# Kernel tuning notes

Hardware: AMD Instinct MI355X
Metric: run time of the kernel (lower is better)

The kernel has to match this reference:

```python
import jax, jax.numpy as jnp
import numpy as np

S, E, K = 100000, 30000, 1000
D, F = 64, 128
B = 16384
NNZ_S, NNZ_E, NNZ_K = 1600000, 480000, 32000
LAYERS = 3
MOMENTUM = 0.9
LEAK = 0.1


def setup_inputs() -> dict:
    key = jax.random.key(0)
    ks = jax.random.split(key, 24)
    inp = {}
    inp['student_id'] = jax.random.randint(ks[0], (B,), 0, S, dtype=jnp.int32)
    inp['exercise_id'] = jax.random.randint(ks[1], (B,), 0, E, dtype=jnp.int32)
    inp['q_mask'] = jnp.ones((B, K), jnp.float32)
    # embedding tables (xavier-ish scale)
    inp['stu_emb'] = jax.random.normal(ks[2], (S, D), jnp.float32) * 0.05
    inp['exer_emb'] = jax.random.normal(ks[3], (E, D), jnp.float32) * 0.05
    inp['know_emb'] = jax.random.normal(ks[4], (K, D), jnp.float32) * 0.05
    inp['impact_emb'] = jax.random.normal(ks[5], (E, D), jnp.float32) * 0.05
    # sparse adjacencies in COO form (rows, cols, vals); vals ~ normalized weights
    inp['s_rows'] = jax.random.randint(ks[6], (NNZ_S,), 0, S, dtype=jnp.int32)
    inp['s_cols'] = jax.random.randint(ks[7], (NNZ_S,), 0, S, dtype=jnp.int32)
    inp['s_vals'] = jax.random.uniform(ks[8], (NNZ_S,), jnp.float32) / 16.0
    inp['e_rows'] = jax.random.randint(ks[9], (NNZ_E,), 0, E, dtype=jnp.int32)
    inp['e_cols'] = jax.random.randint(ks[10], (NNZ_E,), 0, E, dtype=jnp.int32)
    inp['e_vals'] = jax.random.uniform(ks[11], (NNZ_E,), jnp.float32) / 16.0
    inp['k_rows'] = jax.random.randint(ks[12], (NNZ_K,), 0, K, dtype=jnp.int32)
    inp['k_cols'] = jax.random.randint(ks[13], (NNZ_K,), 0, K, dtype=jnp.int32)
    inp['k_vals'] = jax.random.uniform(ks[14], (NNZ_K,), jnp.float32) / 32.0
    # linear layers (stored as [in, out])
    inp['W_stu'] = jax.random.normal(ks[15], (D, F), jnp.float32) * 0.1
    inp['b_stu'] = jnp.zeros((F,), jnp.float32)
    inp['W_exer'] = jax.random.normal(ks[16], (D, F), jnp.float32) * 0.1
    inp['b_exer'] = jnp.zeros((F,), jnp.float32)
    inp['W_know'] = jax.random.normal(ks[17], (D, F), jnp.float32) * 0.1
    inp['b_know'] = jnp.zeros((F,), jnp.float32)
    inp['W_disc'] = jax.random.normal(ks[18], (D, 1), jnp.float32) * 0.1
    inp['b_disc'] = jnp.zeros((1,), jnp.float32)
    return inp


def spmm(rows, cols, vals, x, n):
    # sparse [n,n] @ dense [n,d] via gather + segment_sum
    return jax.ops.segment_sum(vals[:, None] * x[cols], rows, num_segments=n)


def convolution(emb, rows, cols, vals, n):
    # layers of SpMM with momentum residual; mean over all (layers+1) outputs
    acc = emb
    cur = emb
    for _ in range(LAYERS):
        cur = spmm(rows, cols, vals, cur, n) + MOMENTUM * cur
        acc = acc + cur
    return acc / (LAYERS + 1)


def reference(student_id, exercise_id, q_mask, stu_emb, exer_emb, know_emb,
              impact_emb, s_rows, s_cols, s_vals, e_rows, e_cols, e_vals,
              k_rows, k_cols, k_vals, W_stu, b_stu, W_exer, b_exer,
              W_know, b_know, W_disc, b_disc):
    stu_fwd = convolution(stu_emb, s_rows, s_cols, s_vals, S)    # [S, D]
    exer_fwd = convolution(exer_emb, e_rows, e_cols, e_vals, E)  # [E, D]
    know_fwd = convolution(know_emb, k_rows, k_cols, k_vals, K)  # [K, D]

    batch_student = stu_fwd[student_id]    # [B, D]
    batch_exercise = exer_fwd[exercise_id]  # [B, D]

    student_ts = jax.nn.leaky_relu(batch_student @ W_stu + b_stu, LEAK)   # [B, F]
    diff_ts = jax.nn.leaky_relu(batch_exercise @ W_exer + b_exer, LEAK)  # [B, F]
    knowledge_ts = jax.nn.leaky_relu(know_fwd @ W_know + b_know, LEAK)   # [K, F]
    disc_ts = jax.nn.sigmoid(batch_exercise @ W_disc + b_disc)          # [B, 1]

    student_ts = student_ts @ knowledge_ts.T  # [B, K]
    diff_ts = diff_ts @ knowledge_ts.T        # [B, K]
    knowledge_impact_ts = impact_emb[exercise_id]  # [B, D]
    return (student_ts, diff_ts, disc_ts, knowledge_ts, knowledge_impact_ts)
```

## Files before the change

### kernel.cpp

```cpp
#include <hip/hip_runtime.h>
#include <hip/hip_bf16.h>

#define S_N 100000
#define E_N 30000
#define K_N 1000
#define D_K 64
#define F_K 128
#define B_N 16384
#define NNZ_S 1600000
#define NNZ_E 480000
#define NNZ_K 32000
#define NNZ_TOT (NNZ_S + NNZ_E + NNZ_K)

#define NB_S 782
#define NB_E 235
#define NB_K 8
#define NB_TOT (NB_S + NB_E + NB_K)

#define CHUNK 4096
#define SB_S 391
#define SB_E 118
#define SB_K 8
#define SB_TOT (SB_S + SB_E + SB_K)

typedef __attribute__((ext_vector_type(8))) short sh8;
typedef __attribute__((ext_vector_type(4))) float f4;

__device__ inline float b2f(ushort u) { return __uint_as_float((unsigned)u << 16); }
__device__ inline ushort f2b(float f) {
    unsigned u = __float_as_uint(f);
    return (ushort)((u + 0x7fffu + ((u >> 16) & 1u)) >> 16);
}

__global__ void bucket_count(const int* __restrict__ sr, const int* __restrict__ er,
                             const int* __restrict__ kr, int* bcnt_tot) {
    int blk = blockIdx.x;
    const int* rows; int boff, nnz, nb, lblk;
    if (blk < SB_S)            { lblk = blk;              rows = sr; boff = 0;           nnz = NNZ_S; nb = NB_S; }
    else if (blk < SB_S + SB_E){ lblk = blk - SB_S;       rows = er; boff = NB_S;        nnz = NNZ_E; nb = NB_E; }
    else                       { lblk = blk - SB_S - SB_E; rows = kr; boff = NB_S + NB_E; nnz = NNZ_K; nb = NB_K; }
    __shared__ int hist[NB_S];
    int t = threadIdx.x;
    for (int i = t; i < nb; i += 256) hist[i] = 0;
    __syncthreads();
    int start = lblk * CHUNK, end = min(start + CHUNK, nnz);
    for (int i = start + t; i < end; i += 256) atomicAdd(&hist[rows[i] >> 7], 1);
    __syncthreads();
    for (int i = t; i < nb; i += 256) {
        int h = hist[i];
        if (h) atomicAdd(&bcnt_tot[boff + i], h);
    }
}

__global__ void bucket_scan(const int* __restrict__ bcnt_tot, int* bucket_base,
                            int* rp_s, int* rp_e, int* rp_k) {
    __shared__ int sd[256];
    int t = threadIdx.x;
    int v[5]; int s = 0;
    for (int j = 0; j < 5; j++) {
        int idx = t * 5 + j;
        v[j] = (idx < NB_TOT) ? bcnt_tot[idx] : 0;
        s += v[j];
    }
    sd[t] = s; __syncthreads();
    for (int off = 1; off < 256; off <<= 1) {
        int x = (t >= off) ? sd[t - off] : 0;
        __syncthreads();
        sd[t] += x;
        __syncthreads();
    }
    int pre = sd[t] - s;
    for (int j = 0; j < 5; j++) {
        int idx = t * 5 + j;
        if (idx < NB_TOT) {
            int segoff = (idx < NB_S) ? 0 : (idx < NB_S + NB_E) ? NNZ_S : (NNZ_S + NNZ_E);
            bucket_base[idx] = pre - segoff;
            pre += v[j];
        }
    }
    if (t == 0) { rp_s[S_N] = NNZ_S; rp_e[E_N] = NNZ_E; rp_k[K_N] = NNZ_K; }
}

__global__ void stage1_bin(const int* __restrict__ sr, const int* __restrict__ sc,
                           const float* __restrict__ sv,
                           const int* __restrict__ er, const int* __restrict__ ec,
                           const float* __restrict__ ev,
                           const int* __restrict__ kr, const int* __restrict__ kc,
                           const float* __restrict__ kv,
                           const int* __restrict__ bucket_base,
                           int* rsv, int2* stg_s, int2* stg_e, int2* stg_k) {
    int blk = blockIdx.x;
    const int* rows; const int* cols; const float* vals;
    int2* stg; int boff, nnz, nb, lblk;
    if (blk < SB_S) {
        lblk = blk; rows = sr; cols = sc; vals = sv; stg = stg_s;
        boff = 0; nnz = NNZ_S; nb = NB_S;
    } else if (blk < SB_S + SB_E) {
        lblk = blk - SB_S; rows = er; cols = ec; vals = ev; stg = stg_e;
        boff = NB_S; nnz = NNZ_E; nb = NB_E;
    } else {
        lblk = blk - SB_S - SB_E; rows = kr; cols = kc; vals = kv; stg = stg_k;
        boff = NB_S + NB_E; nnz = NNZ_K; nb = NB_K;
    }
    __shared__ int hist[NB_S];
    __shared__ int wbase[NB_S];
    int t = threadIdx.x;
    for (int i = t; i < nb; i += 256) hist[i] = 0;
    __syncthreads();
    int start = lblk * CHUNK, end = min(start + CHUNK, nnz);
    for (int i = start + t; i < end; i += 256) atomicAdd(&hist[rows[i] >> 7], 1);
    __syncthreads();
    for (int i = t; i < nb; i += 256) {
        int h = hist[i];
        int b0 = h ? atomicAdd(&rsv[boff + i], h) : 0;
        wbase[i] = bucket_base[boff + i] + b0;
        hist[i] = 0;
    }
    __syncthreads();
    for (int i = start + t; i < end; i += 256) {
        int r = rows[i]; int b = r >> 7;
        int p = wbase[b] + atomicAdd(&hist[b], 1);
        stg[p] = make_int2(((r & 127) << 25) | cols[i], __float_as_int(vals[i]));
    }
}

__global__ void stage2_place(const int* __restrict__ bucket_base, const int* __restrict__ bcnt_tot,
                             const int2* __restrict__ stg_s, int2* pr_s, int* rp_s,
                             const int2* __restrict__ stg_e, int2* pr_e, int* rp_e,
                             const int2* __restrict__ stg_k, int2* pr_k, int* rp_k) {
    int gb = blockIdx.x;
    int b = gb;
    const int2* stg; int2* pr; int* rp; int len;
    if (b < NB_S) { stg = stg_s; pr = pr_s; rp = rp_s; len = S_N; }
    else if (b < NB_S + NB_E) { b -= NB_S; stg = stg_e; pr = pr_e; rp = rp_e; len = E_N; }
    else { b -= NB_S + NB_E; stg = stg_k; pr = pr_k; rp = rp_k; len = K_N; }
    int r0 = b << 7;
    int rows = min(128, len - r0);
    __shared__ int cnt[128];
    __shared__ int nx[128];
    int t = threadIdx.x;
    if (t < 128) cnt[t] = 0;
    __syncthreads();
    int j0 = bucket_base[gb], j1 = j0 + bcnt_tot[gb];
    for (int j = j0 + t; j < j1; j += 256)
        atomicAdd(&cnt[((unsigned)stg[j].x) >> 25], 1);
    __syncthreads();
    int my = (t < 128) ? cnt[t] : 0;
    for (int off = 1; off < 128; off <<= 1) {
        int y = (t < 128 && t >= off) ? cnt[t - off] : 0;
        __syncthreads();
        if (t < 128) cnt[t] += y;
        __syncthreads();
    }
    if (t < 128) {
        int ex = j0 + cnt[t] - my;
        nx[t] = ex;
        if (t < rows) rp[r0 + t] = ex;
    }
    __syncthreads();
    for (int j = j0 + t; j < j1; j += 256) {
        int2 e = stg[j];
        int r_rel = ((unsigned)e.x) >> 25;
        int col = e.x & 0x01FFFFFF;
        int p = atomicAdd(&nx[r_rel], 1);
        pr[p] = make_int2(col, e.y);
    }
}

__global__ void convert_bf16(const float* __restrict__ a, const float* __restrict__ b,
                             const float* __restrict__ c,
                             ushort* oa, ushort* ob, ushort* oc) {
    const int NA = S_N * 64, NB = E_N * 64, NC = K_N * 64;
    int i = (blockIdx.x * 256 + threadIdx.x) * 4;
    const float* src; ushort* dst;
    if (i < NA) { src = a; dst = oa; }
    else if (i < NA + NB) { i -= NA; src = b; dst = ob; }
    else if (i < NA + NB + NC) { i -= NA + NB; src = c; dst = oc; }
    else return;
    float4 v = *(const float4*)&src[i];
    ushort4 o;
    o.x = f2b(v.x); o.y = f2b(v.y); o.z = f2b(v.z); o.w = f2b(v.w);
    *(ushort4*)&dst[i] = o;
}

__device__ __forceinline__ void spmm_row_compute(
        const int* __restrict__ rp, const int2* __restrict__ pr,
        const ushort* __restrict__ x, int r, int l, float* a) {
    const ushort4* __restrict__ X4 = (const ushort4*)x;
    int j0 = rp[r], j1 = rp[r + 1];
    ushort4 self = X4[r * 16 + l];
    float a0 = 0.9f * b2f(self.x), a1 = 0.9f * b2f(self.y);
    float a2 = 0.9f * b2f(self.z), a3 = 0.9f * b2f(self.w);
    int j = j0;
    for (; j + 8 <= j1; j += 8) {
        int2 q0 = pr[j + 0], q1 = pr[j + 1], q2 = pr[j + 2], q3 = pr[j + 3];
        int2 q4 = pr[j + 4], q5 = pr[j + 5], q6 = pr[j + 6], q7 = pr[j + 7];
        ushort4 v0 = X4[q0.x * 16 + l];
        ushort4 v1 = X4[q1.x * 16 + l];
        ushort4 v2 = X4[q2.x * 16 + l];
        ushort4 v3 = X4[q3.x * 16 + l];
        ushort4 v4 = X4[q4.x * 16 + l];
        ushort4 v5 = X4[q5.x * 16 + l];
        ushort4 v6 = X4[q6.x * 16 + l];
        ushort4 v7 = X4[q7.x * 16 + l];
        float w0 = __int_as_float(q0.y), w1 = __int_as_float(q1.y);
        float w2 = __int_as_float(q2.y), w3 = __int_as_float(q3.y);
        float w4 = __int_as_float(q4.y), w5 = __int_as_float(q5.y);
        float w6 = __int_as_float(q6.y), w7 = __int_as_float(q7.y);
        a0 = fmaf(w0, b2f(v0.x), a0); a1 = fmaf(w0, b2f(v0.y), a1);
        a2 = fmaf(w0, b2f(v0.z), a2); a3 = fmaf(w0, b2f(v0.w), a3);
        a0 = fmaf(w1, b2f(v1.x), a0); a1 = fmaf(w1, b2f(v1.y), a1);
        a2 = fmaf(w1, b2f(v1.z), a2); a3 = fmaf(w1, b2f(v1.w), a3);
        a0 = fmaf(w2, b2f(v2.x), a0); a1 = fmaf(w2, b2f(v2.y), a1);
        a2 = fmaf(w2, b2f(v2.z), a2); a3 = fmaf(w2, b2f(v2.w), a3);
        a0 = fmaf(w3, b2f(v3.x), a0); a1 = fmaf(w3, b2f(v3.y), a1);
        a2 = fmaf(w3, b2f(v3.z), a2); a3 = fmaf(w3, b2f(v3.w), a3);
        a0 = fmaf(w4, b2f(v4.x), a0); a1 = fmaf(w4, b2f(v4.y), a1);
        a2 = fmaf(w4, b2f(v4.z), a2); a3 = fmaf(w4, b2f(v4.w), a3);
        a0 = fmaf(w5, b2f(v5.x), a0); a1 = fmaf(w5, b2f(v5.y), a1);
        a2 = fmaf(w5, b2f(v5.z), a2); a3 = fmaf(w5, b2f(v5.w), a3);
        a0 = fmaf(w6, b2f(v6.x), a0); a1 = fmaf(w6, b2f(v6.y), a1);
        a2 = fmaf(w6, b2f(v6.z), a2); a3 = fmaf(w6, b2f(v6.w), a3);
        a0 = fmaf(w7, b2f(v7.x), a0); a1 = fmaf(w7, b2f(v7.y), a1);
        a2 = fmaf(w7, b2f(v7.z), a2); a3 = fmaf(w7, b2f(v7.w), a3);
    }
    if (j + 4 <= j1) {
        int2 q0 = pr[j + 0], q1 = pr[j + 1], q2 = pr[j + 2], q3 = pr[j + 3];
        ushort4 v0 = X4[q0.x * 16 + l];
        ushort4 v1 = X4[q1.x * 16 + l];
        ushort4 v2 = X4[q2.x * 16 + l];
        ushort4 v3 = X4[q3.x * 16 + l];
        float w0 = __int_as_float(q0.y), w1 = __int_as_float(q1.y);
        float w2 = __int_as_float(q2.y), w3 = __int_as_float(q3.y);
        a0 = fmaf(w0, b2f(v0.x), a0); a1 = fmaf(w0, b2f(v0.y), a1);
        a2 = fmaf(w0, b2f(v0.z), a2); a3 = fmaf(w0, b2f(v0.w), a3);
        a0 = fmaf(w1, b2f(v1.x), a0); a1 = fmaf(w1, b2f(v1.y), a1);
        a2 = fmaf(w1, b2f(v1.z), a2); a3 = fmaf(w1, b2f(v1.w), a3);
        a0 = fmaf(w2, b2f(v2.x), a0); a1 = fmaf(w2, b2f(v2.y), a1);
        a2 = fmaf(w2, b2f(v2.z), a2); a3 = fmaf(w2, b2f(v2.w), a3);
        a0 = fmaf(w3, b2f(v3.x), a0); a1 = fmaf(w3, b2f(v3.y), a1);
        a2 = fmaf(w3, b2f(v3.z), a2); a3 = fmaf(w3, b2f(v3.w), a3);
        j += 4;
    }
    if (j < j1) {
        int last = j1 - 1;
        int2 q0 = pr[j];
        int2 q1 = pr[min(j + 1, last)];
        int2 q2 = pr[min(j + 2, last)];
        int2 q3 = pr[min(j + 3, last)];
        ushort4 v0 = X4[q0.x * 16 + l];
        ushort4 v1 = X4[q1.x * 16 + l];
        ushort4 v2 = X4[q2.x * 16 + l];
        ushort4 v3 = X4[q3.x * 16 + l];
        float w0 = __int_as_float(q0.y);
        float w1 = (j + 1 <= last) ? __int_as_float(q1.y) : 0.f;
        float w2 = (j + 2 <= last) ? __int_as_float(q2.y) : 0.f;
        float w3 = (j + 3 <= last) ? __int_as_float(q3.y) : 0.f;
        a0 = fmaf(w0, b2f(v0.x), a0); a1 = fmaf(w0, b2f(v0.y), a1);
        a2 = fmaf(w0, b2f(v0.z), a2); a3 = fmaf(w0, b2f(v0.w), a3);
        a0 = fmaf(w1, b2f(v1.x), a0); a1 = fmaf(w1, b2f(v1.y), a1);
        a2 = fmaf(w1, b2f(v1.z), a2); a3 = fmaf(w1, b2f(v1.w), a3);
        a0 = fmaf(w2, b2f(v2.x), a0); a1 = fmaf(w2, b2f(v2.y), a1);
        a2 = fmaf(w2, b2f(v2.z), a2); a3 = fmaf(w2, b2f(v2.w), a3);
        a0 = fmaf(w3, b2f(v3.x), a0); a1 = fmaf(w3, b2f(v3.y), a1);
        a2 = fmaf(w3, b2f(v3.z), a2); a3 = fmaf(w3, b2f(v3.w), a3);
    }
    a[0] = a0; a[1] = a1; a[2] = a2; a[3] = a3;
}

__global__ void spmm_full(const int* __restrict__ rp_s, const int2* __restrict__ pr_s,
                          const ushort* __restrict__ xs, ushort* ys,
                          const int* __restrict__ rp_e, const int2* __restrict__ pr_e,
                          const ushort* __restrict__ xe, ushort* ye,
                          const int* __restrict__ rp_k, const int2* __restrict__ pr_k,
                          const ushort* __restrict__ xk, ushort* yk) {
    int w = (blockIdx.x * 256 + threadIdx.x) >> 4;
    int l = threadIdx.x & 15;
    const int* rp; const int2* pr; const ushort* x; ushort* y; int r;
    if (w < S_N) { rp = rp_s; pr = pr_s; x = xs; y = ys; r = w; }
    else if (w < S_N + E_N) { rp = rp_e; pr = pr_e; x = xe; y = ye; r = w - S_N; }
    else if (w < S_N + E_N + K_N) { rp = rp_k; pr = pr_k; x = xk; y = yk; r = w - S_N - E_N; }
    else return;
    float a[4];
    spmm_row_compute(rp, pr, x, r, l, a);
    ushort4 o;
    o.x = f2b(a[0]); o.y = f2b(a[1]); o.z = f2b(a[2]); o.w = f2b(a[3]);
    *(ushort4*)&y[r * 64 + l * 4] = o;
}

__global__ void spmm_last(const int* __restrict__ sid, const int* __restrict__ eid,
                          const int* __restrict__ rp_s, const int2* __restrict__ pr_s,
                          const ushort* __restrict__ xs, ushort* c3s,
                          const int* __restrict__ rp_e, const int2* __restrict__ pr_e,
                          const ushort* __restrict__ xe, ushort* c3e,
                          const int* __restrict__ rp_k, const int2* __restrict__ pr_k,
                          const ushort* __restrict__ xk, ushort* yk) {
    int w = (blockIdx.x * 256 + threadIdx.x) >> 4;
    int l = threadIdx.x & 15;
    const int* rp; const int2* pr; const ushort* x; ushort* y; int r; int orow;
    if (w < B_N) { rp = rp_s; pr = pr_s; x = xs; y = c3s; r = sid[w]; orow = w; }
    else if (w < 2 * B_N) {
        int b = w - B_N;
        rp = rp_e; pr = pr_e; x = xe; y = c3e; r = eid[b]; orow = b;
    } else if (w < 2 * B_N + K_N) {
        r = w - 2 * B_N;
        rp = rp_k; pr = pr_k; x = xk; y = yk; orow = r;
    } else return;
    float a[4];
    spmm_row_compute(rp, pr, x, r, l, a);
    ushort4 o;
    o.x = f2b(a[0]); o.y = f2b(a[1]); o.z = f2b(a[2]); o.w = f2b(a[3]);
    *(ushort4*)&y[orow * 64 + l * 4] = o;
}

__global__ void gather_init(const int* __restrict__ sid, const int* __restrict__ eid,
                            const float* __restrict__ src_s, const float* __restrict__ src_e,
                            const float* __restrict__ src_k,
                            float* bacc_s, float* bacc_e, float* kacc) {
    int i = blockIdx.x * 256 + threadIdx.x;
    const int BD = B_N * 64;
    if (i < BD) {
        int b = i >> 6, d = i & 63;
        bacc_s[i] = src_s[(long)sid[b] * 64 + d];
    } else if (i < 2 * BD) {
        int ii = i - BD; int b = ii >> 6, d = ii & 63;
        bacc_e[ii] = src_e[(long)eid[b] * 64 + d];
    } else if (i < 2 * BD + K_N * 64) {
        int ii = i - 2 * BD;
        kacc[ii] = src_k[ii];
    }
}

__global__ void gather_accb(const int* __restrict__ sid, const int* __restrict__ eid,
                            const ushort* __restrict__ src_s, const ushort* __restrict__ src_e,
                            const ushort* __restrict__ src_k,
                            float* bacc_s, float* bacc_e, float* kacc) {
    int i = blockIdx.x * 256 + threadIdx.x;
    const int BD = B_N * 64;
    if (i < BD) {
        int b = i >> 6, d = i & 63;
        bacc_s[i] += b2f(src_s[(long)sid[b] * 64 + d]);
    } else if (i < 2 * BD) {
        int ii = i - BD; int b = ii >> 6, d = ii & 63;
        bacc_e[ii] += b2f(src_e[(long)eid[b] * 64 + d]);
    } else if (i < 2 * BD + K_N * 64) {
        int ii = i - 2 * BD;
        kacc[ii] += b2f(src_k[ii]);
    }
}

__global__ void dense_mm(const float* __restrict__ bacc_s, const ushort* __restrict__ c3_s,
                         const float* __restrict__ bacc_e, const ushort* __restrict__ c3_e,
                         const float* __restrict__ W_stu, const float* __restrict__ b_stu,
                         const float* __restrict__ W_exer, const float* __restrict__ b_exer,
                         __hip_bfloat16* st_b, __hip_bfloat16* df_b) {
    int which = blockIdx.y;
    const float* bacc = which ? bacc_e : bacc_s;
    const ushort* c3 = which ? c3_e : c3_s;
    const float* W = which ? W_exer : W_stu;
    const float* bias = which ? b_exer : b_stu;
    __hip_bfloat16* out = which ? df_b : st_b;
    int r0 = blockIdx.x * 2;
    int t = threadIdx.x;
    __shared__ float X[2][64];
    if (t < 128) {
        int lr = t >> 6, d = t & 63; int b = r0 + lr;
        X[lr][d] = 0.25f * (bacc[(long)b * 64 + d] + b2f(c3[(long)b * 64 + d]));
    }
    __syncthreads();
    int lr = t >> 7, f = t & 127;
    float acc = bias[f];
    for (int d = 0; d < 64; d++) acc += X[lr][d] * W[d * 128 + f];
    acc = acc > 0.f ? acc : 0.1f * acc;
    out[(long)(r0 + lr) * 128 + f] = __float2bfloat16(acc);
}

__global__ void know_mm(const float* __restrict__ kacc, const ushort* __restrict__ cur3_k,
                        const float* __restrict__ W, const float* __restrict__ bias,
                        float* out_f32, __hip_bfloat16* kn_b) {
    int r0 = blockIdx.x * 2;
    int t = threadIdx.x;
    __shared__ float X[2][64];
    if (t < 128) {
        int lr = t >> 6, d = t & 63; int r = r0 + lr;
        X[lr][d] = (r < K_N) ? 0.25f * (kacc[r * 64 + d] + b2f(cur3_k[r * 64 + d])) : 0.f;
    }
    __syncthreads();
    int lr = t >> 7, f = t & 127; int r = r0 + lr;
    float acc = bias[f];
    for (int d = 0; d < 64; d++) acc += X[lr][d] * W[d * 128 + f];
    acc = acc > 0.f ? acc : 0.1f * acc;
    if (r < K_N) {
        out_f32[(long)r * 128 + f] = acc;
        kn_b[(long)r * 128 + f] = __float2bfloat16(acc);
    } else {
        kn_b[(long)r * 128 + f] = __float2bfloat16(0.f);
    }
}

__global__ void disc_kernel(const float* __restrict__ bacc_e, const ushort* __restrict__ c3_e,
                            const float* __restrict__ W_disc, const float* __restrict__ b_disc,
                            float* out) {
    int w = (blockIdx.x * 256 + threadIdx.x) >> 6;
    int d = threadIdx.x & 63;
    if (w >= B_N) return;
    float x = 0.25f * (bacc_e[(long)w * 64 + d] + b2f(c3_e[(long)w * 64 + d])) * W_disc[d];
    for (int off = 32; off > 0; off >>= 1) x += __shfl_down(x, off, 64);
    if (d == 0) {
        float z = x + b_disc[0];
        out[w] = 1.f / (1.f + expf(-z));
    }
}

__global__ void impact_kernel(const int* __restrict__ eid, const float* __restrict__ imp,
                              float* out) {
    int i = blockIdx.x * 256 + threadIdx.x;
    if (i >= B_N * 64) return;
    int b = i >> 6, d = i & 63;
    out[i] = imp[(long)eid[b] * 64 + d];
}

__global__ void big_mm(const __hip_bfloat16* __restrict__ st, const __hip_bfloat16* __restrict__ df,
                       const __hip_bfloat16* __restrict__ kn,
                       float* __restrict__ out0, float* __restrict__ out1) {
    const ushort* X = (const ushort*)(blockIdx.z ? df : st);
    const ushort* Kn = (const ushort*)kn;
    float* out = blockIdx.z ? out1 : out0;
    int wv = threadIdx.x >> 6;
    int lane = threadIdx.x & 63;
    int m_blk = blockIdx.y * 64 + (wv >> 1) * 32;
    int n_blk = blockIdx.x * 64 + (wv & 1) * 32;
    int q = lane >> 4, l16 = lane & 15;
    f4 acc00 = {0.f, 0.f, 0.f, 0.f}, acc01 = acc00, acc10 = acc00, acc11 = acc00;
    for (int s = 0; s < 4; s++) {
        int kofs = s * 32 + q * 8;
        sh8 a0 = *(const sh8*)&X[(long)(m_blk + l16) * 128 + kofs];
        sh8 a1 = *(const sh8*)&X[(long)(m_blk + 16 + l16) * 128 + kofs];
        sh8 b0 = *(const sh8*)&Kn[(long)(n_blk + l16) * 128 + kofs];
        sh8 b1 = *(const sh8*)&Kn[(long)(n_blk + 16 + l16) * 128 + kofs];
        acc00 = __builtin_amdgcn_mfma_f32_16x16x32_bf16(a0, b0, acc00, 0, 0, 0);
        acc01 = __builtin_amdgcn_mfma_f32_16x16x32_bf16(a0, b1, acc01, 0, 0, 0);
        acc10 = __builtin_amdgcn_mfma_f32_16x16x32_bf16(a1, b0, acc10, 0, 0, 0);
        acc11 = __builtin_amdgcn_mfma_f32_16x16x32_bf16(a1, b1, acc11, 0, 0, 0);
    }
    for (int r = 0; r < 4; r++) {
        int row0 = m_blk + q * 4 + r;
        int row1 = m_blk + 16 + q * 4 + r;
        int col0 = n_blk + l16;
        int col1 = n_blk + 16 + l16;
        if (col0 < K_N) {
            out[(long)row0 * K_N + col0] = acc00[r];
            out[(long)row1 * K_N + col0] = acc10[r];
        }
        if (col1 < K_N) {
            out[(long)row0 * K_N + col1] = acc01[r];
            out[(long)row1 * K_N + col1] = acc11[r];
        }
    }
}

extern "C" void kernel_launch(void* const* d_in, const int* in_sizes, int n_in,
                              void* d_out, int out_size, void* d_ws, size_t ws_size,
                              hipStream_t stream) {
    const int* sid = (const int*)d_in[0];
    const int* eid = (const int*)d_in[1];
    const float* stu_emb = (const float*)d_in[3];
    const float* exer_emb = (const float*)d_in[4];
    const float* know_emb = (const float*)d_in[5];
    const float* impact_emb = (const float*)d_in[6];
    const int* s_rows = (const int*)d_in[7];
    const int* s_cols = (const int*)d_in[8];
    const float* s_vals = (const float*)d_in[9];
    const int* e_rows = (const int*)d_in[10];
    const int* e_cols = (const int*)d_in[11];
    const float* e_vals = (const float*)d_in[12];
    const int* k_rows = (const int*)d_in[13];
    const int* k_cols = (const int*)d_in[14];
    const float* k_vals = (const float*)d_in[15];
    const float* W_stu = (const float*)d_in[16];
    const float* b_stu = (const float*)d_in[17];
    const float* W_exer = (const float*)d_in[18];
    const float* b_exer = (const float*)d_in[19];
    const float* W_know = (const float*)d_in[20];
    const float* b_know = (const float*)d_in[21];
    const float* W_disc = (const float*)d_in[22];
    const float* b_disc = (const float*)d_in[23];

    float* out = (float*)d_out;
    float* out_st = out;
    float* out_df = out + 16384000;
    float* out_disc = out + 32768000;
    float* out_kn = out + 32784384;
    float* out_imp = out + 32912384;

    char* p = (char*)d_ws;
    auto alloc = [&](size_t bytes) -> char* {
        char* r = p;
        p += (bytes + 255) & ~(size_t)255;
        return r;
    };
    ushort* xb_s = (ushort*)alloc((size_t)S_N * 64 * 2);
    ushort* xb_e = (ushort*)alloc((size_t)E_N * 64 * 2);
    ushort* xb_k = (ushort*)alloc((size_t)K_N * 64 * 2);
    ushort* bufA_s = (ushort*)alloc((size_t)S_N * 64 * 2);
    ushort* bufB_s = (ushort*)alloc((size_t)S_N * 64 * 2);
    ushort* bufA_e = (ushort*)alloc((size_t)E_N * 64 * 2);
    ushort* bufB_e = (ushort*)alloc((size_t)E_N * 64 * 2);
    ushort* bufA_k = (ushort*)alloc((size_t)K_N * 64 * 2);
    ushort* bufB_k = (ushort*)alloc((size_t)K_N * 64 * 2);
    ushort* c3s = (ushort*)alloc((size_t)B_N * 64 * 2);
    ushort* c3e = (ushort*)alloc((size_t)B_N * 64 * 2);
    float* bacc_s = (float*)alloc((size_t)B_N * 64 * 4);
    float* bacc_e = (float*)alloc((size_t)B_N * 64 * 4);
    float* kacc = (float*)alloc((size_t)K_N * 64 * 4);
    __hip_bfloat16* st_b = (__hip_bfloat16*)alloc((size_t)B_N * 128 * 2);
    __hip_bfloat16* df_b = (__hip_bfloat16*)alloc((size_t)B_N * 128 * 2);
    __hip_bfloat16* kn_b = (__hip_bfloat16*)alloc((size_t)1024 * 128 * 2);
    int* bcnt_tot = (int*)alloc((size_t)2 * NB_TOT * 4);
    int* rsv = bcnt_tot + NB_TOT;
    int* bucket_base = (int*)alloc((size_t)NB_TOT * 4);
    int* rp_s = (int*)alloc((size_t)(S_N + 1) * 4);
    int* rp_e = (int*)alloc((size_t)(E_N + 1) * 4);
    int* rp_k = (int*)alloc((size_t)(K_N + 1) * 4);
    int2* stg_s = (int2*)alloc((size_t)NNZ_S * 8);
    int2* stg_e = (int2*)alloc((size_t)NNZ_E * 8);
    int2* stg_k = (int2*)alloc((size_t)NNZ_K * 8);
    int2* pr_s = (int2*)alloc((size_t)NNZ_S * 8);
    int2* pr_e = (int2*)alloc((size_t)NNZ_E * 8);
    int2* pr_k = (int2*)alloc((size_t)NNZ_K * 8);

    hipMemsetAsync(bcnt_tot, 0, (size_t)2 * NB_TOT * 4, stream);
    bucket_count<<<SB_TOT, 256, 0, stream>>>(s_rows, e_rows, k_rows, bcnt_tot);
    bucket_scan<<<1, 256, 0, stream>>>(bcnt_tot, bucket_base, rp_s, rp_e, rp_k);
    stage1_bin<<<SB_TOT, 256, 0, stream>>>(
        s_rows, s_cols, s_vals, e_rows, e_cols, e_vals, k_rows, k_cols, k_vals,
        bucket_base, rsv, stg_s, stg_e, stg_k);
    stage2_place<<<NB_TOT, 256, 0, stream>>>(bucket_base, bcnt_tot,
                                             stg_s, pr_s, rp_s,
                                             stg_e, pr_e, rp_e,
                                             stg_k, pr_k, rp_k);

    const int conv_blocks = ((S_N + E_N + K_N) * 64 / 4 + 255) / 256;
    convert_bf16<<<conv_blocks, 256, 0, stream>>>(stu_emb, exer_emb, know_emb, xb_s, xb_e, xb_k);

    const int gather_blocks = (2 * B_N * 64 + K_N * 64) / 256;
    const int full_blocks = ((S_N + E_N + K_N) * 16 + 255) / 256;
    const int last_blocks = ((2 * B_N + K_N) * 16 + 255) / 256;
    gather_init<<<gather_blocks, 256, 0, stream>>>(sid, eid, stu_emb, exer_emb, know_emb,
                                                   bacc_s, bacc_e, kacc);
    spmm_full<<<full_blocks, 256, 0, stream>>>(rp_s, pr_s, xb_s, bufA_s,
                                               rp_e, pr_e, xb_e, bufA_e,
                                               rp_k, pr_k, xb_k, bufA_k);
    gather_accb<<<gather_blocks, 256, 0, stream>>>(sid, eid, bufA_s, bufA_e, bufA_k,
                                                   bacc_s, bacc_e, kacc);
    spmm_full<<<full_blocks, 256, 0, stream>>>(rp_s, pr_s, bufA_s, bufB_s,
                                               rp_e, pr_e, bufA_e, bufB_e,
                                               rp_k, pr_k, bufA_k, bufB_k);
    gather_accb<<<gather_blocks, 256, 0, stream>>>(sid, eid, bufB_s, bufB_e, bufB_k,
                                                   bacc_s, bacc_e, kacc);
    spmm_last<<<last_blocks, 256, 0, stream>>>(sid, eid,
                                               rp_s, pr_s, bufB_s, c3s,
                                               rp_e, pr_e, bufB_e, c3e,
                                               rp_k, pr_k, bufB_k, bufA_k);

    dense_mm<<<dim3(B_N / 2, 2), 256, 0, stream>>>(bacc_s, c3s, bacc_e, c3e,
                                                   W_stu, b_stu, W_exer, b_exer, st_b, df_b);
    know_mm<<<512, 256, 0, stream>>>(kacc, bufA_k, W_know, b_know, out_kn, kn_b);
    disc_kernel<<<B_N / 4, 256, 0, stream>>>(bacc_e, c3e, W_disc, b_disc, out_disc);
    impact_kernel<<<B_N * 64 / 256, 256, 0, stream>>>(eid, impact_emb, out_imp);

    big_mm<<<dim3(16, B_N / 64, 2), 256, 0, stream>>>(st_b, df_b, kn_b, out_st, out_df);
}
```

Measured before the change: 570.6 us.

## Merge independent kernels into horizontally fused launches and drop the scan kernel

Cuts the number of kernel launches by merging independent work into single grids partitioned by block index. Conversion, the initial gathers, the bucket count and the impact gather now run in one pre-kernel. The layer-2 and layer-3 SpMMs each absorb the gather-accumulate of the previous layer, and the dense, knowledge and discrimination kernels become one post-kernel. The global bucket scan kernel is removed: stage1 recomputes a per-segment prefix scan in every block, and stage2 sums the preceding bucket counts itself. This trades redundant scan work and heavier per-block branching for fewer launches and inter-kernel bubbles.

```diff
diff --git a/kernel.cpp b/kernel.cpp
--- a/kernel.cpp
+++ b/kernel.cpp
@@ -23,6 +23,15 @@
 #define SB_K 8
 #define SB_TOT (SB_S + SB_E + SB_K)
 
+#define NCONV 8188
+#define NGATH 8442
+#define NIMP 4096
+#define FULLB 8188
+#define LASTB 2111
+#define NDENSE 16384
+#define NKNOW 512
+#define NDISC 4096
+
 typedef __attribute__((ext_vector_type(8))) short sh8;
 typedef __attribute__((ext_vector_type(4))) float f4;
 
@@ -32,53 +41,63 @@
     return (ushort)((u + 0x7fffu + ((u >> 16) & 1u)) >> 16);
 }
 
-__global__ void bucket_count(const int* __restrict__ sr, const int* __restrict__ er,
-                             const int* __restrict__ kr, int* bcnt_tot) {
+__global__ void pre_kernel(const float* __restrict__ stu_emb, const float* __restrict__ exer_emb,
+                           const float* __restrict__ know_emb,
+                           ushort* xb_s, ushort* xb_e, ushort* xb_k,
+                           const int* __restrict__ sid, const int* __restrict__ eid,
+                           float* bacc_s, float* bacc_e, float* kacc,
+                           const int* __restrict__ sr, const int* __restrict__ er,
+                           const int* __restrict__ kr, int* bcnt_tot,
+                           const float* __restrict__ imp, float* out_imp) {
     int blk = blockIdx.x;
-    const int* rows; int boff, nnz, nb, lblk;
-    if (blk < SB_S)            { lblk = blk;              rows = sr; boff = 0;           nnz = NNZ_S; nb = NB_S; }
-    else if (blk < SB_S + SB_E){ lblk = blk - SB_S;       rows = er; boff = NB_S;        nnz = NNZ_E; nb = NB_E; }
-    else                       { lblk = blk - SB_S - SB_E; rows = kr; boff = NB_S + NB_E; nnz = NNZ_K; nb = NB_K; }
-    __shared__ int hist[NB_S];
     int t = threadIdx.x;
-    for (int i = t; i < nb; i += 256) hist[i] = 0;
-    __syncthreads();
-    int start = lblk * CHUNK, end = min(start + CHUNK, nnz);
-    for (int i = start + t; i < end; i += 256) atomicAdd(&hist[rows[i] >> 7], 1);
-    __syncthreads();
-    for (int i = t; i < nb; i += 256) {
-        int h = hist[i];
-        if (h) atomicAdd(&bcnt_tot[boff + i], h);
-    }
-}
-
-__global__ void bucket_scan(const int* __restrict__ bcnt_tot, int* bucket_base,
-                            int* rp_s, int* rp_e, int* rp_k) {
-    __shared__ int sd[256];
-    int t = threadIdx.x;
-    int v[5]; int s = 0;
-    for (int j = 0; j < 5; j++) {
-        int idx = t * 5 + j;
-        v[j] = (idx < NB_TOT) ? bcnt_tot[idx] : 0;
-        s += v[j];
-    }
-    sd[t] = s; __syncthreads();
-    for (int off = 1; off < 256; off <<= 1) {
-        int x = (t >= off) ? sd[t - off] : 0;
-        __syncthreads();
-        sd[t] += x;
-        __syncthreads();
-    }
-    int pre = sd[t] - s;
-    for (int j = 0; j < 5; j++) {
-        int idx = t * 5 + j;
-        if (idx < NB_TOT) {
-            int segoff = (idx < NB_S) ? 0 : (idx < NB_S + NB_E) ? NNZ_S : (NNZ_S + NNZ_E);
-            bucket_base[idx] = pre - segoff;
-            pre += v[j];
-        }
-    }
-    if (t == 0) { rp_s[S_N] = NNZ_S; rp_e[E_N] = NNZ_E; rp_k[K_N] = NNZ_K; }
+    if (blk < NCONV) {
+        const int NA = S_N * 64, NB = E_N * 64, NC = K_N * 64;
+        int i = (blk * 256 + t) * 4;
+        const float* src; ushort* dst;
+        if (i < NA) { src = stu_emb; dst = xb_s; }
+        else if (i < NA + NB) { i -= NA; src = exer_emb; dst = xb_e; }
+        else if (i < NA + NB + NC) { i -= NA + NB; src = know_emb; dst = xb_k; }
+        else return;
+        float4 v = *(const float4*)&src[i];
+        ushort4 o;
+        o.x = f2b(v.x); o.y = f2b(v.y); o.z = f2b(v.z); o.w = f2b(v.w);
+        *(ushort4*)&dst[i] = o;
+    } else if (blk < NCONV + NGATH) {
+        int i = (blk - NCONV) * 256 + t;
+        const int BD = B_N * 64;
+        if (i < BD) {
+            int b = i >> 6, d = i & 63;
+            bacc_s[i] = stu_emb[(long)sid[b] * 64 + d];
+        } else if (i < 2 * BD) {
+            int ii = i - BD; int b = ii >> 6, d = ii & 63;
+            bacc_e[ii] = exer_emb[(long)eid[b] * 64 + d];
+        } else if (i < 2 * BD + K_N * 64) {
+            int ii = i - 2 * BD;
+            kacc[ii] = know_emb[ii];
+        }
+    } else if (blk < NCONV + NGATH + SB_TOT) {
+        int lb = blk - NCONV - NGATH;
+        const int* rows; int boff, nnz, nb, lblk;
+        if (lb < SB_S)            { lblk = lb;              rows = sr; boff = 0;           nnz = NNZ_S; nb = NB_S; }
+        else if (lb < SB_S + SB_E){ lblk = lb - SB_S;       rows = er; boff = NB_S;        nnz = NNZ_E; nb = NB_E; }
+        else                      { lblk = lb - SB_S - SB_E; rows = kr; boff = NB_S + NB_E; nnz = NNZ_K; nb = NB_K; }
+        __shared__ int hist[NB_S];
+        for (int i = t; i < nb; i += 256) hist[i] = 0;
+        __syncthreads();
+        int start = lblk * CHUNK, end = min(start + CHUNK, nnz);
+        for (int i = start + t; i < end; i += 256) atomicAdd(&hist[rows[i] >> 7], 1);
+        __syncthreads();
+        for (int i = t; i < nb; i += 256) {
+            int h = hist[i];
+            if (h) atomicAdd(&bcnt_tot[boff + i], h);
+        }
+    } else {
+        int i = (blk - NCONV - NGATH - SB_TOT) * 256 + t;
+        if (i >= B_N * 64) return;
+        int b = i >> 6, d = i & 63;
+        out_imp[i] = imp[(long)eid[b] * 64 + d];
+    }
 }
 
 __global__ void stage1_bin(const int* __restrict__ sr, const int* __restrict__ sc,
@@ -87,7 +106,7 @@
                            const float* __restrict__ ev,
                            const int* __restrict__ kr, const int* __restrict__ kc,
                            const float* __restrict__ kv,
-                           const int* __restrict__ bucket_base,
+                           const int* __restrict__ bcnt_tot,
                            int* rsv, int2* stg_s, int2* stg_e, int2* stg_k) {
     int blk = blockIdx.x;
     const int* rows; const int* cols; const float* vals;
@@ -104,7 +123,27 @@
     }
     __shared__ int hist[NB_S];
     __shared__ int wbase[NB_S];
+    __shared__ int base_l[NB_S];
+    __shared__ int sc_s[256];
     int t = threadIdx.x;
+    int lv[4]; int ls = 0;
+    for (int j = 0; j < 4; j++) {
+        int idx = t * 4 + j;
+        lv[j] = (idx < nb) ? bcnt_tot[boff + idx] : 0;
+        ls += lv[j];
+    }
+    sc_s[t] = ls; __syncthreads();
+    for (int off = 1; off < 256; off <<= 1) {
+        int x = (t >= off) ? sc_s[t - off] : 0;
+        __syncthreads();
+        sc_s[t] += x;
+        __syncthreads();
+    }
+    int pre = sc_s[t] - ls;
+    for (int j = 0; j < 4; j++) {
+        int idx = t * 4 + j;
+        if (idx < nb) { base_l[idx] = pre; pre += lv[j]; }
+    }
     for (int i = t; i < nb; i += 256) hist[i] = 0;
     __syncthreads();
     int start = lblk * CHUNK, end = min(start + CHUNK, nnz);
@@ -113,7 +152,7 @@
     for (int i = t; i < nb; i += 256) {
         int h = hist[i];
         int b0 = h ? atomicAdd(&rsv[boff + i], h) : 0;
-        wbase[i] = bucket_base[boff + i] + b0;
+        wbase[i] = base_l[i] + b0;
         hist[i] = 0;
     }
     __syncthreads();
@@ -124,24 +163,34 @@
     }
 }
 
-__global__ void stage2_place(const int* __restrict__ bucket_base, const int* __restrict__ bcnt_tot,
+__global__ void stage2_place(const int* __restrict__ bcnt_tot,
                              const int2* __restrict__ stg_s, int2* pr_s, int* rp_s,
                              const int2* __restrict__ stg_e, int2* pr_e, int* rp_e,
                              const int2* __restrict__ stg_k, int2* pr_k, int* rp_k) {
     int gb = blockIdx.x;
     int b = gb;
-    const int2* stg; int2* pr; int* rp; int len;
-    if (b < NB_S) { stg = stg_s; pr = pr_s; rp = rp_s; len = S_N; }
-    else if (b < NB_S + NB_E) { b -= NB_S; stg = stg_e; pr = pr_e; rp = rp_e; len = E_N; }
-    else { b -= NB_S + NB_E; stg = stg_k; pr = pr_k; rp = rp_k; len = K_N; }
+    const int2* stg; int2* pr; int* rp; int len, segbase, segnnz;
+    if (b < NB_S) { stg = stg_s; pr = pr_s; rp = rp_s; len = S_N; segbase = 0; segnnz = NNZ_S; }
+    else if (b < NB_S + NB_E) { b -= NB_S; stg = stg_e; pr = pr_e; rp = rp_e; len = E_N; segbase = NB_S; segnnz = NNZ_E; }
+    else { b -= NB_S + NB_E; stg = stg_k; pr = pr_k; rp = rp_k; len = K_N; segbase = NB_S + NB_E; segnnz = NNZ_K; }
     int r0 = b << 7;
     int rows = min(128, len - r0);
     __shared__ int cnt[128];
     __shared__ int nx[128];
+    __shared__ int red[256];
     int t = threadIdx.x;
+    int s = 0;
+    for (int i = t; i < b; i += 256) s += bcnt_tot[segbase + i];
+    red[t] = s;
     if (t < 128) cnt[t] = 0;
     __syncthreads();
-    int j0 = bucket_base[gb], j1 = j0 + bcnt_tot[gb];
+    for (int off = 128; off > 0; off >>= 1) {
+        if (t < off) red[t] += red[t + off];
+        __syncthreads();
+    }
+    int j0 = red[0];
+    int j1 = j0 + bcnt_tot[segbase + b];
+    if (b == 0 && t == 0) rp[len] = segnnz;
     for (int j = j0 + t; j < j1; j += 256)
         atomicAdd(&cnt[((unsigned)stg[j].x) >> 25], 1);
     __syncthreads();
@@ -165,22 +214,6 @@
         int p = atomicAdd(&nx[r_rel], 1);
         pr[p] = make_int2(col, e.y);
     }
-}
-
-__global__ void convert_bf16(const float* __restrict__ a, const float* __restrict__ b,
-                             const float* __restrict__ c,
-                             ushort* oa, ushort* ob, ushort* oc) {
-    const int NA = S_N * 64, NB = E_N * 64, NC = K_N * 64;
-    int i = (blockIdx.x * 256 + threadIdx.x) * 4;
-    const float* src; ushort* dst;
-    if (i < NA) { src = a; dst = oa; }
-    else if (i < NA + NB) { i -= NA; src = b; dst = ob; }
-    else if (i < NA + NB + NC) { i -= NA + NB; src = c; dst = oc; }
-    else return;
-    float4 v = *(const float4*)&src[i];
-    ushort4 o;
-    o.x = f2b(v.x); o.y = f2b(v.y); o.z = f2b(v.z); o.w = f2b(v.w);
-    *(ushort4*)&dst[i] = o;
 }
 
 __device__ __forceinline__ void spmm_row_compute(
@@ -268,14 +301,16 @@
     a[0] = a0; a[1] = a1; a[2] = a2; a[3] = a3;
 }
 
-__global__ void spmm_full(const int* __restrict__ rp_s, const int2* __restrict__ pr_s,
-                          const ushort* __restrict__ xs, ushort* ys,
-                          const int* __restrict__ rp_e, const int2* __restrict__ pr_e,
-                          const ushort* __restrict__ xe, ushort* ye,
-                          const int* __restrict__ rp_k, const int2* __restrict__ pr_k,
-                          const ushort* __restrict__ xk, ushort* yk) {
-    int w = (blockIdx.x * 256 + threadIdx.x) >> 4;
-    int l = threadIdx.x & 15;
+__device__ __forceinline__ void spmm_full_body(
+        int blk0, int t,
+        const int* __restrict__ rp_s, const int2* __restrict__ pr_s,
+        const ushort* __restrict__ xs, ushort* ys,
+        const int* __restrict__ rp_e, const int2* __restrict__ pr_e,
+        const ushort* __restrict__ xe, ushort* ye,
+        const int* __restrict__ rp_k, const int2* __restrict__ pr_k,
+        const ushort* __restrict__ xk, ushort* yk) {
+    int w = (blk0 * 256 + t) >> 4;
+    int l = t & 15;
     const int* rp; const int2* pr; const ushort* x; ushort* y; int r;
     if (w < S_N) { rp = rp_s; pr = pr_s; x = xs; y = ys; r = w; }
     else if (w < S_N + E_N) { rp = rp_e; pr = pr_e; x = xe; y = ye; r = w - S_N; }
@@ -288,54 +323,11 @@
     *(ushort4*)&y[r * 64 + l * 4] = o;
 }
 
-__global__ void spmm_last(const int* __restrict__ sid, const int* __restrict__ eid,
-                          const int* __restrict__ rp_s, const int2* __restrict__ pr_s,
-                          const ushort* __restrict__ xs, ushort* c3s,
-                          const int* __restrict__ rp_e, const int2* __restrict__ pr_e,
-                          const ushort* __restrict__ xe, ushort* c3e,
-                          const int* __restrict__ rp_k, const int2* __restrict__ pr_k,
-                          const ushort* __restrict__ xk, ushort* yk) {
-    int w = (blockIdx.x * 256 + threadIdx.x) >> 4;
-    int l = threadIdx.x & 15;
-    const int* rp; const int2* pr; const ushort* x; ushort* y; int r; int orow;
-    if (w < B_N) { rp = rp_s; pr = pr_s; x = xs; y = c3s; r = sid[w]; orow = w; }
-    else if (w < 2 * B_N) {
-        int b = w - B_N;
-        rp = rp_e; pr = pr_e; x = xe; y = c3e; r = eid[b]; orow = b;
-    } else if (w < 2 * B_N + K_N) {
-        r = w - 2 * B_N;
-        rp = rp_k; pr = pr_k; x = xk; y = yk; orow = r;
-    } else return;
-    float a[4];
-    spmm_row_compute(rp, pr, x, r, l, a);
-    ushort4 o;
-    o.x = f2b(a[0]); o.y = f2b(a[1]); o.z = f2b(a[2]); o.w = f2b(a[3]);
-    *(ushort4*)&y[orow * 64 + l * 4] = o;
-}
-
-__global__ void gather_init(const int* __restrict__ sid, const int* __restrict__ eid,
-                            const float* __restrict__ src_s, const float* __restrict__ src_e,
-                            const float* __restrict__ src_k,
-                            float* bacc_s, float* bacc_e, float* kacc) {
-    int i = blockIdx.x * 256 + threadIdx.x;
-    const int BD = B_N * 64;
-    if (i < BD) {
-        int b = i >> 6, d = i & 63;
-        bacc_s[i] = src_s[(long)sid[b] * 64 + d];
-    } else if (i < 2 * BD) {
-        int ii = i - BD; int b = ii >> 6, d = ii & 63;
-        bacc_e[ii] = src_e[(long)eid[b] * 64 + d];
-    } else if (i < 2 * BD + K_N * 64) {
-        int ii = i - 2 * BD;
-        kacc[ii] = src_k[ii];
-    }
-}
-
-__global__ void gather_accb(const int* __restrict__ sid, const int* __restrict__ eid,
-                            const ushort* __restrict__ src_s, const ushort* __restrict__ src_e,
-                            const ushort* __restrict__ src_k,
-                            float* bacc_s, float* bacc_e, float* kacc) {
-    int i = blockIdx.x * 256 + threadIdx.x;
+__device__ __forceinline__ void gather_accb_body(
+        int i, const int* __restrict__ sid, const int* __restrict__ eid,
+        const ushort* __restrict__ src_s, const ushort* __restrict__ src_e,
+        const ushort* __restrict__ src_k,
+        float* bacc_s, float* bacc_e, float* kacc) {
     const int BD = B_N * 64;
     if (i < BD) {
         int b = i >> 6, d = i & 63;
@@ -349,75 +341,128 @@
     }
 }
 
-__global__ void dense_mm(const float* __restrict__ bacc_s, const ushort* __restrict__ c3_s,
-                         const float* __restrict__ bacc_e, const ushort* __restrict__ c3_e,
-                         const float* __restrict__ W_stu, const float* __restrict__ b_stu,
-                         const float* __restrict__ W_exer, const float* __restrict__ b_exer,
-                         __hip_bfloat16* st_b, __hip_bfloat16* df_b) {
-    int which = blockIdx.y;
-    const float* bacc = which ? bacc_e : bacc_s;
-    const ushort* c3 = which ? c3_e : c3_s;
-    const float* W = which ? W_exer : W_stu;
-    const float* bias = which ? b_exer : b_stu;
-    __hip_bfloat16* out = which ? df_b : st_b;
-    int r0 = blockIdx.x * 2;
+__global__ void spmm_l1(const int* __restrict__ rp_s, const int2* __restrict__ pr_s,
+                        const ushort* __restrict__ xs, ushort* ys,
+                        const int* __restrict__ rp_e, const int2* __restrict__ pr_e,
+                        const ushort* __restrict__ xe, ushort* ye,
+                        const int* __restrict__ rp_k, const int2* __restrict__ pr_k,
+                        const ushort* __restrict__ xk, ushort* yk) {
+    spmm_full_body(blockIdx.x, threadIdx.x, rp_s, pr_s, xs, ys,
+                   rp_e, pr_e, xe, ye, rp_k, pr_k, xk, yk);
+}
+
+__global__ void spmm_l2_fused(const int* __restrict__ rp_s, const int2* __restrict__ pr_s,
+                              const ushort* __restrict__ xs, ushort* ys,
+                              const int* __restrict__ rp_e, const int2* __restrict__ pr_e,
+                              const ushort* __restrict__ xe, ushort* ye,
+                              const int* __restrict__ rp_k, const int2* __restrict__ pr_k,
+                              const ushort* __restrict__ xk, ushort* yk,
+                              const int* __restrict__ sid, const int* __restrict__ eid,
+                              float* bacc_s, float* bacc_e, float* kacc) {
+    int blk = blockIdx.x;
+    if (blk < FULLB) {
+        spmm_full_body(blk, threadIdx.x, rp_s, pr_s, xs, ys,
+                       rp_e, pr_e, xe, ye, rp_k, pr_k, xk, yk);
+    } else {
+        int i = (blk - FULLB) * 256 + threadIdx.x;
+        gather_accb_body(i, sid, eid, xs, xe, xk, bacc_s, bacc_e, kacc);
+    }
+}
+
+__global__ void spmm_l3_fused(const int* __restrict__ sid, const int* __restrict__ eid,
+                              const int* __restrict__ rp_s, const int2* __restrict__ pr_s,
+                              const ushort* __restrict__ xs, ushort* c3s,
+                              const int* __restrict__ rp_e, const int2* __restrict__ pr_e,
+                              const ushort* __restrict__ xe, ushort* c3e,
+                              const int* __restrict__ rp_k, const int2* __restrict__ pr_k,
+                              const ushort* __restrict__ xk, ushort* yk,
+                              float* bacc_s, float* bacc_e, float* kacc) {
+    int blk = blockIdx.x;
     int t = threadIdx.x;
-    __shared__ float X[2][64];
-    if (t < 128) {
-        int lr = t >> 6, d = t & 63; int b = r0 + lr;
-        X[lr][d] = 0.25f * (bacc[(long)b * 64 + d] + b2f(c3[(long)b * 64 + d]));
-    }
-    __syncthreads();
-    int lr = t >> 7, f = t & 127;
-    float acc = bias[f];
-    for (int d = 0; d < 64; d++) acc += X[lr][d] * W[d * 128 + f];
-    acc = acc > 0.f ? acc : 0.1f * acc;
-    out[(long)(r0 + lr) * 128 + f] = __float2bfloat16(acc);
-}
-
-__global__ void know_mm(const float* __restrict__ kacc, const ushort* __restrict__ cur3_k,
-                        const float* __restrict__ W, const float* __restrict__ bias,
-                        float* out_f32, __hip_bfloat16* kn_b) {
-    int r0 = blockIdx.x * 2;
+    if (blk < LASTB) {
+        int w = (blk * 256 + t) >> 4;
+        int l = t & 15;
+        const int* rp; const int2* pr; const ushort* x; ushort* y; int r; int orow;
+        if (w < B_N) { rp = rp_s; pr = pr_s; x = xs; y = c3s; r = sid[w]; orow = w; }
+        else if (w < 2 * B_N) {
+            int b = w - B_N;
+            rp = rp_e; pr = pr_e; x = xe; y = c3e; r = eid[b]; orow = b;
+        } else if (w < 2 * B_N + K_N) {
+            r = w - 2 * B_N;
+            rp = rp_k; pr = pr_k; x = xk; y = yk; orow = r;
+        } else return;
+        float a[4];
+        spmm_row_compute(rp, pr, x, r, l, a);
+        ushort4 o;
+        o.x = f2b(a[0]); o.y = f2b(a[1]); o.z = f2b(a[2]); o.w = f2b(a[3]);
+        *(ushort4*)&y[orow * 64 + l * 4] = o;
+    } else {
+        int i = (blk - LASTB) * 256 + t;
+        gather_accb_body(i, sid, eid, xs, xe, xk, bacc_s, bacc_e, kacc);
+    }
+}
+
+__global__ void post_kernel(const float* __restrict__ bacc_s, const ushort* __restrict__ c3_s,
+                            const float* __restrict__ bacc_e, const ushort* __restrict__ c3_e,
+                            const float* __restrict__ W_stu, const float* __restrict__ b_stu,
+                            const float* __restrict__ W_exer, const float* __restrict__ b_exer,
+                            __hip_bfloat16* st_b, __hip_bfloat16* df_b,
+                            const float* __restrict__ kacc, const ushort* __restrict__ cur3_k,
+                            const float* __restrict__ W_know, const float* __restrict__ b_know,
+                            float* out_kn_f32, __hip_bfloat16* kn_b,
+                            const float* __restrict__ W_disc, const float* __restrict__ b_disc,
+                            float* out_disc) {
+    int blk = blockIdx.x;
     int t = threadIdx.x;
-    __shared__ float X[2][64];
-    if (t < 128) {
-        int lr = t >> 6, d = t & 63; int r = r0 + lr;
-        X[lr][d] = (r < K_N) ? 0.25f * (kacc[r * 64 + d] + b2f(cur3_k[r * 64 + d])) : 0.f;
-    }
-    __syncthreads();
-    int lr = t >> 7, f = t & 127; int r = r0 + lr;
-    float acc = bias[f];
-    for (int d = 0; d < 64; d++) acc += X[lr][d] * W[d * 128 + f];
-    acc = acc > 0.f ? acc : 0.1f * acc;
-    if (r < K_N) {
-        out_f32[(long)r * 128 + f] = acc;
-        kn_b[(long)r * 128 + f] = __float2bfloat16(acc);
+    if (blk < NDENSE) {
+        int which = blk >> 13;
+        int local = blk & 8191;
+        const float* bacc = which ? bacc_e : bacc_s;
+        const ushort* c3 = which ? c3_e : c3_s;
+        const float* W = which ? W_exer : W_stu;
+        const float* bias = which ? b_exer : b_stu;
+        __hip_bfloat16* out = which ? df_b : st_b;
+        int r0 = local * 2;
+        __shared__ float X[2][64];
+        if (t < 128) {
+            int lr = t >> 6, d = t & 63; int b = r0 + lr;
+            X[lr][d] = 0.25f * (bacc[(long)b * 64 + d] + b2f(c3[(long)b * 64 + d]));
+        }
+        __syncthreads();
+        int lr = t >> 7, f = t & 127;
+        float acc = bias[f];
+        for (int d = 0; d < 64; d++) acc += X[lr][d] * W[d * 128 + f];
+        acc = acc > 0.f ? acc : 0.1f * acc;
+        out[(long)(r0 + lr) * 128 + f] = __float2bfloat16(acc);
+    } else if (blk < NDENSE + NKNOW) {
+        int r0 = (blk - NDENSE) * 2;
+        __shared__ float X[2][64];
+        if (t < 128) {
+            int lr = t >> 6, d = t & 63; int r = r0 + lr;
+            X[lr][d] = (r < K_N) ? 0.25f * (kacc[r * 64 + d] + b2f(cur3_k[r * 64 + d])) : 0.f;
+        }
+        __syncthreads();
+        int lr = t >> 7, f = t & 127; int r = r0 + lr;
+        float acc = b_know[f];
+        for (int d = 0; d < 64; d++) acc += X[lr][d] * W_know[d * 128 + f];
+        acc = acc > 0.f ? acc : 0.1f * acc;
+        if (r < K_N) {
+            out_kn_f32[(long)r * 128 + f] = acc;
+            kn_b[(long)r * 128 + f] = __float2bfloat16(acc);
+        } else {
+            kn_b[(long)r * 128 + f] = __float2bfloat16(0.f);
+        }
     } else {
-        kn_b[(long)r * 128 + f] = __float2bfloat16(0.f);
-    }
-}
-
-__global__ void disc_kernel(const float* __restrict__ bacc_e, const ushort* __restrict__ c3_e,
-                            const float* __restrict__ W_disc, const float* __restrict__ b_disc,
-                            float* out) {
-    int w = (blockIdx.x * 256 + threadIdx.x) >> 6;
-    int d = threadIdx.x & 63;
-    if (w >= B_N) return;
-    float x = 0.25f * (bacc_e[(long)w * 64 + d] + b2f(c3_e[(long)w * 64 + d])) * W_disc[d];
-    for (int off = 32; off > 0; off >>= 1) x += __shfl_down(x, off, 64);
-    if (d == 0) {
-        float z = x + b_disc[0];
-        out[w] = 1.f / (1.f + expf(-z));
-    }
-}
-
-__global__ void impact_kernel(const int* __restrict__ eid, const float* __restrict__ imp,
-                              float* out) {
-    int i = blockIdx.x * 256 + threadIdx.x;
-    if (i >= B_N * 64) return;
-    int b = i >> 6, d = i & 63;
-    out[i] = imp[(long)eid[b] * 64 + d];
+        int w = ((blk - NDENSE - NKNOW) * 256 + t) >> 6;
+        int d = t & 63;
+        if (w >= B_N) return;
+        float x = 0.25f * (bacc_e[(long)w * 64 + d] + b2f(c3_e[(long)w * 64 + d])) * W_disc[d];
+        for (int off = 32; off > 0; off >>= 1) x += __shfl_down(x, off, 64);
+        if (d == 0) {
+            float z = x + b_disc[0];
+            out_disc[w] = 1.f / (1.f + expf(-z));
+        }
+    }
 }
 
 __global__ void big_mm(const __hip_bfloat16* __restrict__ st, const __hip_bfloat16* __restrict__ df,
@@ -518,7 +563,6 @@
     __hip_bfloat16* kn_b = (__hip_bfloat16*)alloc((size_t)1024 * 128 * 2);
     int* bcnt_tot = (int*)alloc((size_t)2 * NB_TOT * 4);
     int* rsv = bcnt_tot + NB_TOT;
-    int* bucket_base = (int*)alloc((size_t)NB_TOT * 4);
     int* rp_s = (int*)alloc((size_t)(S_N + 1) * 4);
     int* rp_e = (int*)alloc((size_t)(E_N + 1) * 4);
     int* rp_k = (int*)alloc((size_t)(K_N + 1) * 4);
@@ -530,44 +574,34 @@
     int2* pr_k = (int2*)alloc((size_t)NNZ_K * 8);
 
     hipMemsetAsync(bcnt_tot, 0, (size_t)2 * NB_TOT * 4, stream);
-    bucket_count<<<SB_TOT, 256, 0, stream>>>(s_rows, e_rows, k_rows, bcnt_tot);
-    bucket_scan<<<1, 256, 0, stream>>>(bcnt_tot, bucket_base, rp_s, rp_e, rp_k);
+    pre_kernel<<<NCONV + NGATH + SB_TOT + NIMP, 256, 0, stream>>>(
+        stu_emb, exer_emb, know_emb, xb_s, xb_e, xb_k,
+        sid, eid, bacc_s, bacc_e, kacc,
+        s_rows, e_rows, k_rows, bcnt_tot, impact_emb, out_imp);
     stage1_bin<<<SB_TOT, 256, 0, stream>>>(
         s_rows, s_cols, s_vals, e_rows, e_cols, e_vals, k_rows, k_cols, k_vals,
-        bucket_base, rsv, stg_s, stg_e, stg_k);
-    stage2_place<<<NB_TOT, 256, 0, stream>>>(bucket_base, bcnt_tot,
+        bcnt_tot, rsv, stg_s, stg_e, stg_k);
+    stage2_place<<<NB_TOT, 256, 0, stream>>>(bcnt_tot,
                                              stg_s, pr_s, rp_s,
                                              stg_e, pr_e, rp_e,
                                              stg_k, pr_k, rp_k);
-
-    const int conv_blocks = ((S_N + E_N + K_N) * 64 / 4 + 255) / 256;
-    convert_bf16<<<conv_blocks, 256, 0, stream>>>(stu_emb, exer_emb, know_emb, xb_s, xb_e, xb_k);
-
-    const int gather_blocks = (2 * B_N * 64 + K_N * 64) / 256;
-    const int full_blocks = ((S_N + E_N + K_N) * 16 + 255) / 256;
-    const int last_blocks = ((2 * B_N + K_N) * 16 + 255) / 256;
-    gather_init<<<gather_blocks, 256, 0, stream>>>(sid, eid, stu_emb, exer_emb, know_emb,
-                                                   bacc_s, bacc_e, kacc);
-    spmm_full<<<full_blocks, 256, 0, stream>>>(rp_s, pr_s, xb_s, bufA_s,
-                                               rp_e, pr_e, xb_e, bufA_e,
-                                               rp_k, pr_k, xb_k, bufA_k);
-    gather_accb<<<gather_blocks, 256, 0, stream>>>(sid, eid, bufA_s, bufA_e, bufA_k,
-                                                   bacc_s, bacc_e, kacc);
-    spmm_full<<<full_blocks, 256, 0, stream>>>(rp_s, pr_s, bufA_s, bufB_s,
-                                               rp_e, pr_e, bufA_e, bufB_e,
-                                               rp_k, pr_k, bufA_k, bufB_k);
-    gather_accb<<<gather_blocks, 256, 0, stream>>>(sid, eid, bufB_s, bufB_e, bufB_k,
-                                                   bacc_s, bacc_e, kacc);
-    spmm_last<<<last_blocks, 256, 0, stream>>>(sid, eid,
-                                               rp_s, pr_s, bufB_s, c3s,
-                                               rp_e, pr_e, bufB_e, c3e,
-                                               rp_k, pr_k, bufB_k, bufA_k);
-
-    dense_mm<<<dim3(B_N / 2, 2), 256, 0, stream>>>(bacc_s, c3s, bacc_e, c3e,
-                                                   W_stu, b_stu, W_exer, b_exer, st_b, df_b);
-    know_mm<<<512, 256, 0, stream>>>(kacc, bufA_k, W_know, b_know, out_kn, kn_b);
-    disc_kernel<<<B_N / 4, 256, 0, stream>>>(bacc_e, c3e, W_disc, b_disc, out_disc);
-    impact_kernel<<<B_N * 64 / 256, 256, 0, stream>>>(eid, impact_emb, out_imp);
-
+    spmm_l1<<<FULLB, 256, 0, stream>>>(rp_s, pr_s, xb_s, bufA_s,
+                                       rp_e, pr_e, xb_e, bufA_e,
+                                       rp_k, pr_k, xb_k, bufA_k);
+    spmm_l2_fused<<<FULLB + NGATH, 256, 0, stream>>>(
+        rp_s, pr_s, bufA_s, bufB_s,
+        rp_e, pr_e, bufA_e, bufB_e,
+        rp_k, pr_k, bufA_k, bufB_k,
+        sid, eid, bacc_s, bacc_e, kacc);
+    spmm_l3_fused<<<LASTB + NGATH, 256, 0, stream>>>(
+        sid, eid,
+        rp_s, pr_s, bufB_s, c3s,
+        rp_e, pr_e, bufB_e, c3e,
+        rp_k, pr_k, bufB_k, bufA_k,
+        bacc_s, bacc_e, kacc);
+    post_kernel<<<NDENSE + NKNOW + NDISC, 256, 0, stream>>>(
+        bacc_s, c3s, bacc_e, c3e, W_stu, b_stu, W_exer, b_exer, st_b, df_b,
+        kacc, bufA_k, W_know, b_know, out_kn, kn_b,
+        W_disc, b_disc, out_disc);
     big_mm<<<dim3(16, B_N / 64, 2), 256, 0, stream>>>(st_b, df_b, kn_b, out_st, out_df);
 }
```

After: 545.6 us. -4.4%, faster.
